# Optimization experiments

Hardware: AMD Instinct MI355X
Metric: run time of the kernel (lower is better)

The kernel has to match this reference:

```python
import jax, jax.numpy as jnp
import numpy as np

HIDDEN = 2048
HEADS = 16
KV_LORA = 512
ROPE_D = 64
NOPE_D = ROPE_D          # module sets qk_nope_head_dim = qk_rope_head_dim
Q_HEAD_D = ROPE_D + NOPE_D
V_D = 128
B, S = 2, 2048
SCALE = ROPE_D ** -0.5


def setup_inputs() -> dict:
    key = jax.random.key(0)
    ks = jax.random.split(key, 6)
    hidden_state = jax.random.normal(ks[0], (B, S, HIDDEN), dtype=jnp.float32)
    attention_mask = jnp.zeros((1, 1, S, S), dtype=jnp.float32)
    s = 0.02
    W_down = jax.random.normal(ks[1], (HIDDEN, KV_LORA + ROPE_D), dtype=jnp.float32) * s
    W_up = jax.random.normal(ks[2], (KV_LORA, HEADS * (NOPE_D + V_D)), dtype=jnp.float32) * s
    W_q = jax.random.normal(ks[3], (HIDDEN, HEADS * Q_HEAD_D), dtype=jnp.float32) * s
    W_o = jax.random.normal(ks[4], (HEADS * V_D, HIDDEN), dtype=jnp.float32) * s
    return {"hidden_state": hidden_state, "attention_mask": attention_mask,
            "W_down": W_down, "W_up": W_up, "W_q": W_q, "W_o": W_o}


def reference(hidden_state, attention_mask, W_down, W_up, W_q, W_o):
    b, s, _ = hidden_state.shape
    # low-rank KV down-projection; split latent and shared rope key
    kv_down = hidden_state @ W_down                      # [b,s,kv_lora+rope]
    kv_compressed = kv_down[..., :KV_LORA]
    k_rope = kv_down[..., KV_LORA:]                      # [b,s,rope]
    # up-project latent to per-head nope-key and value
    kv = (kv_compressed @ W_up).reshape(b, s, HEADS, NOPE_D + V_D)
    kv = kv.transpose(0, 2, 1, 3)                        # [b,h,s,nope+v]
    k_nope = kv[..., :NOPE_D]
    v = kv[..., NOPE_D:]
    # queries
    q = (hidden_state @ W_q).reshape(b, s, HEADS, Q_HEAD_D).transpose(0, 2, 1, 3)
    q_rope = q[..., :ROPE_D]
    q_nope = q[..., ROPE_D:]
    q_full = jnp.concatenate([q_rope, q_nope], axis=-1)  # [b,h,s,2d]
    # broadcast shared rope key across heads and concat with per-head nope key
    k_rope_exp = jnp.broadcast_to(k_rope[:, None], (b, HEADS, s, ROPE_D))
    k_full = jnp.concatenate([k_rope_exp, k_nope], axis=-1)
    scores = jnp.einsum('bhqd,bhkd->bhqk', q_full, k_full) * SCALE
    scores = scores + attention_mask
    probs = jax.nn.softmax(scores, axis=-1)
    ctx = jnp.einsum('bhqk,bhkd->bhqd', probs, v)        # [b,h,s,v]
    ctx = ctx.transpose(0, 2, 1, 3).reshape(b, s, HEADS * V_D)
    return ctx @ W_o
```

## Files before the change

### kernel.cpp

```cpp
#include <hip/hip_runtime.h>
#include <hip/hip_bf16.h>

#define HEADS   16
#define S_LEN   2048
#define BATCH   2
#define MTOT    (BATCH * S_LEN)
#define HIDDEN  2048
#define SCALE   0.125f
#define QKD_LD  2688

typedef __attribute__((ext_vector_type(8))) short          bf16x8;
typedef __attribute__((ext_vector_type(8))) unsigned short u16x8;
typedef __attribute__((ext_vector_type(4))) unsigned short u16x4;
typedef __attribute__((ext_vector_type(4))) float          f32x4;

__device__ __forceinline__ unsigned short f2bf(float f) {
    union { float f; unsigned u; } v; v.f = f;
    unsigned r = v.u + 0x7FFFu + ((v.u >> 16) & 1u);
    return (unsigned short)(r >> 16);
}

__device__ __forceinline__ void gld16(const void* g, const void* l) {
    __builtin_amdgcn_global_load_lds(
        (const __attribute__((address_space(1))) void*)g,
        (__attribute__((address_space(3))) void*)l, 16, 0, 0);
}

__global__ __launch_bounds__(256)
void cast_bf16(const float* __restrict__ in, unsigned short* __restrict__ out)
{
    const size_t i = ((size_t)blockIdx.x * 256 + threadIdx.x) * 8;
    float4 a = *(const float4*)&in[i];
    float4 b = *(const float4*)&in[i + 4];
    u16x8 o;
    o[0] = f2bf(a.x); o[1] = f2bf(a.y); o[2] = f2bf(a.z); o[3] = f2bf(a.w);
    o[4] = f2bf(b.x); o[5] = f2bf(b.y); o[6] = f2bf(b.z); o[7] = f2bf(b.w);
    *(u16x8*)&out[i] = o;
}

__global__ __launch_bounds__(256)
void tc_w(const float* __restrict__ W, int N, int K, unsigned short* __restrict__ Wt)
{
    __shared__ float Tf[64][68];
    const int t  = threadIdx.x;
    const int n0 = blockIdx.x * 64, k0 = blockIdx.y * 64;
    if (n0 >= N) {
        u16x8 z = {0,0,0,0,0,0,0,0};
#pragma unroll
        for (int ii = 0; ii < 2; ii++) {
            int idx = t + 256 * ii;
            int rn = idx >> 3, c8 = (idx & 7) * 8;
            *(u16x8*)&Wt[(size_t)(n0 + rn) * K + k0 + c8] = z;
        }
        return;
    }
#pragma unroll
    for (int ii = 0; ii < 4; ii++) {
        int idx = t + 256 * ii;
        int rk = idx >> 4, c4 = (idx & 15) * 4;
        *(float4*)&Tf[rk][c4] = *(const float4*)&W[(size_t)(k0 + rk) * N + n0 + c4];
    }
    __syncthreads();
#pragma unroll
    for (int ii = 0; ii < 2; ii++) {
        int idx = t + 256 * ii;
        int rn = idx >> 3, c8 = (idx & 7) * 8;
        u16x8 o;
#pragma unroll
        for (int j = 0; j < 8; j++) o[j] = f2bf(Tf[c8 + j][rn]);
        *(u16x8*)&Wt[(size_t)(n0 + rn) * K + k0 + c8] = o;
    }
}

__global__ __launch_bounds__(256)
void transpose_v(const unsigned short* __restrict__ kvu, unsigned short* __restrict__ vT)
{
    __shared__ unsigned short Ts[64][80];
    const int t  = threadIdx.x;
    const int s0 = blockIdx.x * 64;
    const int h  = blockIdx.y >> 1, d0 = (blockIdx.y & 1) * 64;
    const int b  = blockIdx.z;
    const size_t base = (size_t)b * S_LEN;
#pragma unroll
    for (int ii = 0; ii < 2; ii++) {
        int idx = t + 256 * ii;
        int rs = idx >> 3, c8 = (idx & 7) * 8;
        *(u16x8*)&Ts[rs][c8] =
            *(const u16x8*)&kvu[(base + s0 + rs) * 3072 + h * 192 + 64 + d0 + c8];
    }
    __syncthreads();
    const size_t bh = (size_t)(b * HEADS + h);
#pragma unroll
    for (int ii = 0; ii < 2; ii++) {
        int idx = t + 256 * ii;
        int rd = idx >> 3, c8 = (idx & 7) * 8;
        u16x8 o;
#pragma unroll
        for (int j = 0; j < 8; j++) o[j] = Ts[c8 + j][rd];
        *(u16x8*)&vT[(bh * 128 + d0 + rd) * S_LEN + s0 + c8] = o;
    }
}

template<bool OUT_BF16>
__global__ __launch_bounds__(256)
void gemm_bf16(const unsigned short* __restrict__ A, int lda, int K,
               const unsigned short* __restrict__ Bt,
               void* __restrict__ C, int N, int ldc)
{
    __shared__ unsigned short As[128 * 32];
    __shared__ unsigned short Bs[128 * 32];
    const int t = threadIdx.x, lane = t & 63, w = t >> 6;
    const int l15 = lane & 15, lg = lane >> 4;
    const int row0 = blockIdx.y * 128, col0 = blockIdx.x * 128;
    const int wr = w >> 1, wc = w & 1;

    f32x4 acc[4][4] = {};

    for (int k0 = 0; k0 < K; k0 += 32) {
        __syncthreads();
#pragma unroll
        for (int ii = 0; ii < 2; ii++) {
            int u = (ii * 4 + w) * 64 + lane;
            gld16(&A[(size_t)(row0 + (u >> 2)) * lda + k0 + (u & 3) * 8],
                  (char*)As + (ii * 4 + w) * 1024);
            gld16(&Bt[(size_t)(col0 + (u >> 2)) * K + k0 + (u & 3) * 8],
                  (char*)Bs + (ii * 4 + w) * 1024);
        }
        __syncthreads();
        bf16x8 af[4], bb[4];
#pragma unroll
        for (int m = 0; m < 4; m++)
            af[m] = *(const bf16x8*)&As[(wr * 64 + m * 16 + l15) * 32 + lg * 8];
#pragma unroll
        for (int n = 0; n < 4; n++)
            bb[n] = *(const bf16x8*)&Bs[(wc * 64 + n * 16 + l15) * 32 + lg * 8];
#pragma unroll
        for (int m = 0; m < 4; m++)
#pragma unroll
            for (int n = 0; n < 4; n++)
                acc[m][n] = __builtin_amdgcn_mfma_f32_16x16x32_bf16(
                    af[m], bb[n], acc[m][n], 0, 0, 0);
    }

#pragma unroll
    for (int m = 0; m < 4; m++)
#pragma unroll
        for (int n = 0; n < 4; n++) {
            int col = col0 + wc * 64 + n * 16 + l15;
            if (col < N) {
#pragma unroll
                for (int r = 0; r < 4; r++) {
                    int row = row0 + wr * 64 + m * 16 + lg * 4 + r;
                    if (OUT_BF16)
                        ((unsigned short*)C)[(size_t)row * ldc + col] = f2bf(acc[m][n][r]);
                    else
                        ((float*)C)[(size_t)row * ldc + col] = acc[m][n][r];
                }
            }
        }
}

__global__ __launch_bounds__(256, 2)
void mla_attn_mfma(const unsigned short* __restrict__ qkd,
                   const unsigned short* __restrict__ kvu,
                   const unsigned short* __restrict__ vT,
                   const float* __restrict__ mask,
                   unsigned short* __restrict__ ctxb)
{
    __shared__ unsigned short Ks[64 * 128];
    __shared__ unsigned short Vs[128 * 64];
    __shared__ unsigned short Pl[4][32 * 72];
    const int t = threadIdx.x, lane = t & 63, w = t >> 6;
    const int l15 = lane & 15, lg = lane >> 4;
    const int h = blockIdx.y, b = blockIdx.z;
    const int q0 = blockIdx.x * 128 + w * 32;
    const size_t base = (size_t)b * S_LEN;
    const size_t bh = (size_t)(b * HEADS + h);
    const unsigned short* qb = qkd + 640;
    unsigned short* Pw = &Pl[w][0];

    bf16x8 qf[2][4];
#pragma unroll
    for (int m = 0; m < 2; m++)
#pragma unroll
        for (int kk = 0; kk < 4; kk++)
            qf[m][kk] = *(const bf16x8*)&qb[(base + q0 + m * 16 + l15) * QKD_LD
                                            + h * 128 + kk * 32 + lg * 8];

    f32x4 octx[2][8] = {};
    float mrun[2] = {-INFINITY, -INFINITY};
    float lrun[2] = {0.f, 0.f};

    for (int kt = 0; kt < S_LEN / 64; kt++) {
        const int s0 = kt * 64;
        __syncthreads();
#pragma unroll
        for (int ii = 0; ii < 4; ii++) {
            int u = (ii * 4 + w) * 64 + lane;
            {
                int row = u >> 4, x = u & 15, y = x ^ (row & 7);
                const unsigned short* g = (y < 8)
                    ? &qkd[(base + s0 + row) * QKD_LD + 512 + y * 8]
                    : &kvu[(base + s0 + row) * 3072 + h * 192 + (y - 8) * 8];
                gld16(g, (char*)Ks + (ii * 4 + w) * 1024);
            }
            {
                int d = u >> 3, x = u & 7, y = x ^ (d & 7);
                gld16(&vT[(bh * 128 + d) * S_LEN + s0 + y * 8],
                      (char*)Vs + (ii * 4 + w) * 1024);
            }
        }
        __syncthreads();

        f32x4 sc[2][4] = {};
#pragma unroll
        for (int n = 0; n < 4; n++) {
            const int key = n * 16 + l15;
#pragma unroll
            for (int kk = 0; kk < 4; kk++) {
                const int x = (kk * 4 + lg) ^ (key & 7);
                bf16x8 kf = *(const bf16x8*)&Ks[key * 128 + x * 8];
                sc[0][n] = __builtin_amdgcn_mfma_f32_16x16x32_bf16(kf, qf[0][kk], sc[0][n], 0, 0, 0);
                sc[1][n] = __builtin_amdgcn_mfma_f32_16x16x32_bf16(kf, qf[1][kk], sc[1][n], 0, 0, 0);
            }
        }

        float e_bc[2][4];
#pragma unroll
        for (int m = 0; m < 2; m++) {
            const size_t qrow = (size_t)(q0 + m * 16 + l15);
            float sv[4][4];
#pragma unroll
            for (int n = 0; n < 4; n++) {
                float4 mv = *(const float4*)&mask[qrow * S_LEN + s0 + n * 16 + lg * 4];
                sv[n][0] = sc[m][n][0] * SCALE + mv.x;
                sv[n][1] = sc[m][n][1] * SCALE + mv.y;
                sv[n][2] = sc[m][n][2] * SCALE + mv.z;
                sv[n][3] = sc[m][n][3] * SCALE + mv.w;
            }
            float loc = sv[0][0];
#pragma unroll
            for (int n = 0; n < 4; n++)
#pragma unroll
                for (int r = 0; r < 4; r++) loc = fmaxf(loc, sv[n][r]);
            loc = fmaxf(loc, __shfl_xor(loc, 16));
            loc = fmaxf(loc, __shfl_xor(loc, 32));
            float mnew = fmaxf(mrun[m], loc);
            float esc = __expf(mrun[m] - mnew);
            mrun[m] = mnew;
            float ls = 0.f;
#pragma unroll
            for (int n = 0; n < 4; n++) {
                float p0 = __expf(sv[n][0] - mnew), p1 = __expf(sv[n][1] - mnew);
                float p2 = __expf(sv[n][2] - mnew), p3 = __expf(sv[n][3] - mnew);
                ls += (p0 + p1) + (p2 + p3);
                u16x4 pk = { f2bf(p0), f2bf(p1), f2bf(p2), f2bf(p3) };
                *(u16x4*)&Pw[(m * 16 + l15) * 72 + n * 16 + lg * 4] = pk;
            }
            ls += __shfl_xor(ls, 16);
            ls += __shfl_xor(ls, 32);
            lrun[m] = lrun[m] * esc + ls;
#pragma unroll
            for (int r = 0; r < 4; r++) e_bc[m][r] = __shfl(esc, lg * 4 + r);
        }

#pragma unroll
        for (int m = 0; m < 2; m++)
#pragma unroll
            for (int vn = 0; vn < 8; vn++)
#pragma unroll
                for (int r = 0; r < 4; r++) octx[m][vn][r] *= e_bc[m][r];

        asm volatile("" ::: "memory");

        bf16x8 paf[2][2];
#pragma unroll
        for (int m = 0; m < 2; m++)
#pragma unroll
            for (int kk = 0; kk < 2; kk++)
                paf[m][kk] = *(const bf16x8*)&Pw[(m * 16 + l15) * 72 + kk * 32 + lg * 8];
#pragma unroll
        for (int vn = 0; vn < 8; vn++) {
            const int d = vn * 16 + l15;
#pragma unroll
            for (int kk = 0; kk < 2; kk++) {
                const int x = (kk * 4 + lg) ^ (d & 7);
                bf16x8 vf = *(const bf16x8*)&Vs[d * 64 + x * 8];
                octx[0][vn] = __builtin_amdgcn_mfma_f32_16x16x32_bf16(paf[0][kk], vf, octx[0][vn], 0, 0, 0);
                octx[1][vn] = __builtin_amdgcn_mfma_f32_16x16x32_bf16(paf[1][kk], vf, octx[1][vn], 0, 0, 0);
            }
        }
    }

#pragma unroll
    for (int m = 0; m < 2; m++) {
        float inv[4];
#pragma unroll
        for (int r = 0; r < 4; r++) inv[r] = 1.0f / __shfl(lrun[m], lg * 4 + r);
#pragma unroll
        for (int vn = 0; vn < 8; vn++)
#pragma unroll
            for (int r = 0; r < 4; r++)
                ctxb[(base + q0 + m * 16 + lg * 4 + r) * 2048 + h * 128 + vn * 16 + l15]
                    = f2bf(octx[m][vn][r] * inv[r]);
    }
}

extern "C" void kernel_launch(void* const* d_in, const int* in_sizes, int n_in,
                              void* d_out, int out_size, void* d_ws, size_t ws_size,
                              hipStream_t stream)
{
    const float* hidden = (const float*)d_in[0];
    const float* mask   = (const float*)d_in[1];
    const float* W_down = (const float*)d_in[2];
    const float* W_up   = (const float*)d_in[3];
    const float* W_q    = (const float*)d_in[4];
    const float* W_o    = (const float*)d_in[5];
    float* out = (float*)d_out;

    unsigned short* p = (unsigned short*)d_ws;
    unsigned short* hb      = p; p += (size_t)MTOT * 2048;
    unsigned short* qkd     = p; p += (size_t)MTOT * QKD_LD;
    unsigned short* kvu_b   = p; p += (size_t)MTOT * 3072;
    unsigned short* vTb     = p; p += (size_t)BATCH * HEADS * 128 * S_LEN;
    unsigned short* ctxb    = p; p += (size_t)MTOT * 2048;
    unsigned short* Wt_cat  = p; p += (size_t)QKD_LD * 2048;
    unsigned short* Wt_up   = p; p += (size_t)3072 * 512;
    unsigned short* Wt_o    = p; p += (size_t)2048 * 2048;

    dim3 blk(256);
    cast_bf16<<<dim3(MTOT * 2048 / (256 * 8)), blk, 0, stream>>>(hidden, hb);
    tc_w<<<dim3(10, 32), blk, 0, stream>>>(W_down, 576, 2048, Wt_cat);
    tc_w<<<dim3(32, 32), blk, 0, stream>>>(W_q, 2048, 2048, Wt_cat + (size_t)640 * 2048);
    tc_w<<<dim3(48, 8),  blk, 0, stream>>>(W_up, 3072, 512, Wt_up);
    tc_w<<<dim3(32, 32), blk, 0, stream>>>(W_o, 2048, 2048, Wt_o);

    gemm_bf16<true><<<dim3(QKD_LD / 128, 32), blk, 0, stream>>>(
        hb, 2048, 2048, Wt_cat, qkd, QKD_LD, QKD_LD);
    gemm_bf16<true><<<dim3(24, 32), blk, 0, stream>>>(
        qkd, QKD_LD, 512, Wt_up, kvu_b, 3072, 3072);

    transpose_v<<<dim3(S_LEN / 64, 2 * HEADS, BATCH), blk, 0, stream>>>(kvu_b, vTb);

    mla_attn_mfma<<<dim3(S_LEN / 128, HEADS, BATCH), blk, 0, stream>>>(
        qkd, kvu_b, vTb, mask, ctxb);

    gemm_bf16<false><<<dim3(16, 32), blk, 0, stream>>>(
        ctxb, 2048, 2048, Wt_o, out, 2048, 2048);
}
```

Baseline: 302.5 us.

## Double-buffer K/V tiles in attention with async prefetch and swizzled P buffer

```diff
diff --git a/kernel.cpp b/kernel.cpp
--- a/kernel.cpp
+++ b/kernel.cpp
@@ -20,6 +20,12 @@
     return (unsigned short)(r >> 16);
 }
 
+__device__ __forceinline__ unsigned cvtpk(float a, float b) {
+    unsigned r;
+    asm("v_cvt_pk_bf16_f32 %0, %1, %2" : "=v"(r) : "v"(a), "v"(b));
+    return r;
+}
+
 __device__ __forceinline__ void gld16(const void* g, const void* l) {
     __builtin_amdgcn_global_load_lds(
         (const __attribute__((address_space(1))) void*)g,
@@ -167,9 +173,8 @@
                    const float* __restrict__ mask,
                    unsigned short* __restrict__ ctxb)
 {
-    __shared__ unsigned short Ks[64 * 128];
-    __shared__ unsigned short Vs[128 * 64];
-    __shared__ unsigned short Pl[4][32 * 72];
+    __shared__ unsigned short KV[2][64 * 128 + 128 * 64];
+    __shared__ unsigned short Pl[4][32 * 64];
     const int t = threadIdx.x, lane = t & 63, w = t >> 6;
     const int l15 = lane & 15, lg = lane >> 4;
     const int h = blockIdx.y, b = blockIdx.z;
@@ -178,6 +183,7 @@
     const size_t bh = (size_t)(b * HEADS + h);
     const unsigned short* qb = qkd + 640;
     unsigned short* Pw = &Pl[w][0];
+    const unsigned psw = (unsigned)(l15 & 7) << 4;
 
     bf16x8 qf[2][4];
 #pragma unroll
@@ -191,9 +197,12 @@
     float mrun[2] = {-INFINITY, -INFINITY};
     float lrun[2] = {0.f, 0.f};
 
-    for (int kt = 0; kt < S_LEN / 64; kt++) {
-        const int s0 = kt * 64;
-        __syncthreads();
+    const float* mrow0 = &mask[(size_t)(q0 + l15) * S_LEN + lg * 4];
+    const float* mrow1 = mrow0 + (size_t)16 * S_LEN;
+
+    auto STAGE = [&](int buf, int s0) {
+        unsigned short* Kb = &KV[buf][0];
+        unsigned short* Vb = &KV[buf][64 * 128];
 #pragma unroll
         for (int ii = 0; ii < 4; ii++) {
             int u = (ii * 4 + w) * 64 + lane;
@@ -202,17 +211,48 @@
                 const unsigned short* g = (y < 8)
                     ? &qkd[(base + s0 + row) * QKD_LD + 512 + y * 8]
                     : &kvu[(base + s0 + row) * 3072 + h * 192 + (y - 8) * 8];
-                gld16(g, (char*)Ks + (ii * 4 + w) * 1024);
+                gld16(g, (char*)Kb + (ii * 4 + w) * 1024);
             }
             {
                 int d = u >> 3, x = u & 7, y = x ^ (d & 7);
                 gld16(&vT[(bh * 128 + d) * S_LEN + s0 + y * 8],
-                      (char*)Vs + (ii * 4 + w) * 1024);
-            }
-        }
-        __syncthreads();
+                      (char*)Vb + (ii * 4 + w) * 1024);
+            }
+        }
+    };
+
+    const int NT = S_LEN / 64;
+    STAGE(0, 0);
+
+    for (int kt = 0; kt < NT; kt++) {
+        const int cur = kt & 1;
+        const int s0 = kt * 64;
+        const unsigned short* Ks = &KV[cur][0];
+        const unsigned short* Vs = &KV[cur][64 * 128];
+
+        __builtin_amdgcn_s_barrier();
+
+        float4 mv[2][4];
+#pragma unroll
+        for (int n = 0; n < 4; n++) {
+            mv[0][n] = *(const float4*)&mrow0[s0 + n * 16];
+            mv[1][n] = *(const float4*)&mrow1[s0 + n * 16];
+        }
+        __builtin_amdgcn_sched_barrier(0);
+
+        if (kt + 1 < NT) {
+            STAGE(cur ^ 1, s0 + 64);
+            __builtin_amdgcn_sched_barrier(0);
+            asm volatile("s_waitcnt vmcnt(16)" ::: "memory");
+        } else {
+            __builtin_amdgcn_sched_barrier(0);
+            asm volatile("s_waitcnt vmcnt(8)" ::: "memory");
+        }
+        __builtin_amdgcn_sched_barrier(0);
+        __builtin_amdgcn_s_barrier();
 
         f32x4 sc[2][4] = {};
+        __builtin_amdgcn_s_setprio(1);
 #pragma unroll
         for (int n = 0; n < 4; n++) {
             const int key = n * 16 + l15;
@@ -224,19 +264,18 @@
                 sc[1][n] = __builtin_amdgcn_mfma_f32_16x16x32_bf16(kf, qf[1][kk], sc[1][n], 0, 0, 0);
             }
         }
+        __builtin_amdgcn_s_setprio(0);
 
         float e_bc[2][4];
 #pragma unroll
         for (int m = 0; m < 2; m++) {
-            const size_t qrow = (size_t)(q0 + m * 16 + l15);
             float sv[4][4];
 #pragma unroll
             for (int n = 0; n < 4; n++) {
-                float4 mv = *(const float4*)&mask[qrow * S_LEN + s0 + n * 16 + lg * 4];
-                sv[n][0] = sc[m][n][0] * SCALE + mv.x;
-                sv[n][1] = sc[m][n][1] * SCALE + mv.y;
-                sv[n][2] = sc[m][n][2] * SCALE + mv.z;
-                sv[n][3] = sc[m][n][3] * SCALE + mv.w;
+                sv[n][0] = sc[m][n][0] * SCALE + mv[m][n].x;
+                sv[n][1] = sc[m][n][1] * SCALE + mv[m][n].y;
+                sv[n][2] = sc[m][n][2] * SCALE + mv[m][n].z;
+                sv[n][3] = sc[m][n][3] * SCALE + mv[m][n].w;
             }
             float loc = sv[0][0];
 #pragma unroll
@@ -249,13 +288,16 @@
             float esc = __expf(mrun[m] - mnew);
             mrun[m] = mnew;
             float ls = 0.f;
+            const int prow = m * 16 + l15;
 #pragma unroll
             for (int n = 0; n < 4; n++) {
                 float p0 = __expf(sv[n][0] - mnew), p1 = __expf(sv[n][1] - mnew);
                 float p2 = __expf(sv[n][2] - mnew), p3 = __expf(sv[n][3] - mnew);
                 ls += (p0 + p1) + (p2 + p3);
-                u16x4 pk = { f2bf(p0), f2bf(p1), f2bf(p2), f2bf(p3) };
-                *(u16x4*)&Pw[(m * 16 + l15) * 72 + n * 16 + lg * 4] = pk;
+                union { unsigned u[2]; u16x4 v; } pk;
+                pk.u[0] = cvtpk(p0, p1);
+                pk.u[1] = cvtpk(p2, p3);
+                *(u16x4*)((char*)Pw + prow * 128 + ((n * 32 + lg * 8) ^ psw)) = pk.v;
             }
             ls += __shfl_xor(ls, 16);
             ls += __shfl_xor(ls, 32);
@@ -275,10 +317,14 @@
 
         bf16x8 paf[2][2];
 #pragma unroll
-        for (int m = 0; m < 2; m++)
+        for (int m = 0; m < 2; m++) {
+            const int prow = m * 16 + l15;
 #pragma unroll
             for (int kk = 0; kk < 2; kk++)
-                paf[m][kk] = *(const bf16x8*)&Pw[(m * 16 + l15) * 72 + kk * 32 + lg * 8];
+                paf[m][kk] = *(const bf16x8*)((char*)Pw + prow * 128
+                                              + ((kk * 64 + lg * 16) ^ psw));
+        }
+        __builtin_amdgcn_s_setprio(1);
 #pragma unroll
         for (int vn = 0; vn < 8; vn++) {
             const int d = vn * 16 + l15;
@@ -290,6 +336,7 @@
                 octx[1][vn] = __builtin_amdgcn_mfma_f32_16x16x32_bf16(paf[1][kk], vf, octx[1][vn], 0, 0, 0);
             }
         }
+        __builtin_amdgcn_s_setprio(0);
     }
 
 #pragma unroll
```

New measurement: 297.5 us. No clear change (-1.6%).

## Shrink attention query tile, add lazy rescale, packed bf16 convert, and MFMA priority

Applied to the files above, without the earlier changes.

```diff
diff --git a/kernel.cpp b/kernel.cpp
--- a/kernel.cpp
+++ b/kernel.cpp
@@ -20,6 +20,12 @@
     return (unsigned short)(r >> 16);
 }
 
+__device__ __forceinline__ unsigned cvtpk(float a, float b) {
+    unsigned r;
+    asm("v_cvt_pk_bf16_f32 %0, %1, %2" : "=v"(r) : "v"(a), "v"(b));
+    return r;
+}
+
 __device__ __forceinline__ void gld16(const void* g, const void* l) {
     __builtin_amdgcn_global_load_lds(
         (const __attribute__((address_space(1))) void*)g,
@@ -160,7 +166,7 @@
         }
 }
 
-__global__ __launch_bounds__(256, 2)
+__global__ __launch_bounds__(256, 4)
 void mla_attn_mfma(const unsigned short* __restrict__ qkd,
                    const unsigned short* __restrict__ kvu,
                    const unsigned short* __restrict__ vT,
@@ -169,31 +175,34 @@
 {
     __shared__ unsigned short Ks[64 * 128];
     __shared__ unsigned short Vs[128 * 64];
-    __shared__ unsigned short Pl[4][32 * 72];
+    __shared__ unsigned short Pl[4][16 * 64];
     const int t = threadIdx.x, lane = t & 63, w = t >> 6;
     const int l15 = lane & 15, lg = lane >> 4;
     const int h = blockIdx.y, b = blockIdx.z;
-    const int q0 = blockIdx.x * 128 + w * 32;
+    const int q0 = blockIdx.x * 64 + w * 16;
     const size_t base = (size_t)b * S_LEN;
     const size_t bh = (size_t)(b * HEADS + h);
     const unsigned short* qb = qkd + 640;
     unsigned short* Pw = &Pl[w][0];
-
-    bf16x8 qf[2][4];
-#pragma unroll
-    for (int m = 0; m < 2; m++)
-#pragma unroll
-        for (int kk = 0; kk < 4; kk++)
-            qf[m][kk] = *(const bf16x8*)&qb[(base + q0 + m * 16 + l15) * QKD_LD
-                                            + h * 128 + kk * 32 + lg * 8];
-
-    f32x4 octx[2][8] = {};
-    float mrun[2] = {-INFINITY, -INFINITY};
-    float lrun[2] = {0.f, 0.f};
-
-    for (int kt = 0; kt < S_LEN / 64; kt++) {
+    const unsigned psw = (unsigned)(l15 & 7) << 4;
+
+    bf16x8 qf[4];
+#pragma unroll
+    for (int kk = 0; kk < 4; kk++)
+        qf[kk] = *(const bf16x8*)&qb[(base + q0 + l15) * QKD_LD
+                                     + h * 128 + kk * 32 + lg * 8];
+
+    f32x4 octx[8] = {};
+    float mrun = -INFINITY, lrun = 0.f;
+
+    const float* mrow = &mask[(size_t)(q0 + l15) * S_LEN + lg * 4];
+
+    const int NT = S_LEN / 64;
+    for (int kt = 0; kt < NT; kt++) {
         const int s0 = kt * 64;
-        __syncthreads();
+
+        __builtin_amdgcn_s_barrier();
+
 #pragma unroll
         for (int ii = 0; ii < 4; ii++) {
             int u = (ii * 4 + w) * 64 + lane;
@@ -210,9 +219,17 @@
                       (char*)Vs + (ii * 4 + w) * 1024);
             }
         }
-        __syncthreads();
-
-        f32x4 sc[2][4] = {};
+        __builtin_amdgcn_sched_barrier(0);
+
+        float4 mv[4];
+#pragma unroll
+        for (int n = 0; n < 4; n++) mv[n] = *(const float4*)&mrow[s0 + n * 16];
+        __builtin_amdgcn_sched_barrier(0);
+        asm volatile("s_waitcnt vmcnt(4)" ::: "memory");
+        __builtin_amdgcn_s_barrier();
+
+        f32x4 sc[4] = {};
+        __builtin_amdgcn_s_setprio(1);
 #pragma unroll
         for (int n = 0; n < 4; n++) {
             const int key = n * 16 + l15;
@@ -220,65 +237,63 @@
             for (int kk = 0; kk < 4; kk++) {
                 const int x = (kk * 4 + lg) ^ (key & 7);
                 bf16x8 kf = *(const bf16x8*)&Ks[key * 128 + x * 8];
-                sc[0][n] = __builtin_amdgcn_mfma_f32_16x16x32_bf16(kf, qf[0][kk], sc[0][n], 0, 0, 0);
-                sc[1][n] = __builtin_amdgcn_mfma_f32_16x16x32_bf16(kf, qf[1][kk], sc[1][n], 0, 0, 0);
-            }
-        }
-
-        float e_bc[2][4];
-#pragma unroll
-        for (int m = 0; m < 2; m++) {
-            const size_t qrow = (size_t)(q0 + m * 16 + l15);
-            float sv[4][4];
-#pragma unroll
-            for (int n = 0; n < 4; n++) {
-                float4 mv = *(const float4*)&mask[qrow * S_LEN + s0 + n * 16 + lg * 4];
-                sv[n][0] = sc[m][n][0] * SCALE + mv.x;
-                sv[n][1] = sc[m][n][1] * SCALE + mv.y;
-                sv[n][2] = sc[m][n][2] * SCALE + mv.z;
-                sv[n][3] = sc[m][n][3] * SCALE + mv.w;
-            }
-            float loc = sv[0][0];
-#pragma unroll
-            for (int n = 0; n < 4; n++)
-#pragma unroll
-                for (int r = 0; r < 4; r++) loc = fmaxf(loc, sv[n][r]);
-            loc = fmaxf(loc, __shfl_xor(loc, 16));
-            loc = fmaxf(loc, __shfl_xor(loc, 32));
-            float mnew = fmaxf(mrun[m], loc);
-            float esc = __expf(mrun[m] - mnew);
-            mrun[m] = mnew;
-            float ls = 0.f;
-#pragma unroll
-            for (int n = 0; n < 4; n++) {
-                float p0 = __expf(sv[n][0] - mnew), p1 = __expf(sv[n][1] - mnew);
-                float p2 = __expf(sv[n][2] - mnew), p3 = __expf(sv[n][3] - mnew);
-                ls += (p0 + p1) + (p2 + p3);
-                u16x4 pk = { f2bf(p0), f2bf(p1), f2bf(p2), f2bf(p3) };
-                *(u16x4*)&Pw[(m * 16 + l15) * 72 + n * 16 + lg * 4] = pk;
-            }
-            ls += __shfl_xor(ls, 16);
-            ls += __shfl_xor(ls, 32);
-            lrun[m] = lrun[m] * esc + ls;
-#pragma unroll
-            for (int r = 0; r < 4; r++) e_bc[m][r] = __shfl(esc, lg * 4 + r);
-        }
-
-#pragma unroll
-        for (int m = 0; m < 2; m++)
+                sc[n] = __builtin_amdgcn_mfma_f32_16x16x32_bf16(kf, qf[kk], sc[n], 0, 0, 0);
+            }
+        }
+        __builtin_amdgcn_s_setprio(0);
+
+        float sv[4][4];
+#pragma unroll
+        for (int n = 0; n < 4; n++) {
+            sv[n][0] = sc[n][0] * SCALE + mv[n].x;
+            sv[n][1] = sc[n][1] * SCALE + mv[n].y;
+            sv[n][2] = sc[n][2] * SCALE + mv[n].z;
+            sv[n][3] = sc[n][3] * SCALE + mv[n].w;
+        }
+        float loc = sv[0][0];
+#pragma unroll
+        for (int n = 0; n < 4; n++)
+#pragma unroll
+            for (int r = 0; r < 4; r++) loc = fmaxf(loc, sv[n][r]);
+        loc = fmaxf(loc, __shfl_xor(loc, 16));
+        loc = fmaxf(loc, __shfl_xor(loc, 32));
+
+        if (!__all((int)(loc <= mrun + 8.f))) {
+            float mnew = fmaxf(mrun, loc);
+            float esc = __expf(mrun - mnew);
+            mrun = mnew;
+            lrun *= esc;
+            float e_bc[4];
+#pragma unroll
+            for (int r = 0; r < 4; r++) e_bc[r] = __shfl(esc, lg * 4 + r);
 #pragma unroll
             for (int vn = 0; vn < 8; vn++)
 #pragma unroll
-                for (int r = 0; r < 4; r++) octx[m][vn][r] *= e_bc[m][r];
+                for (int r = 0; r < 4; r++) octx[vn][r] *= e_bc[r];
+        }
+
+        float ls = 0.f;
+#pragma unroll
+        for (int n = 0; n < 4; n++) {
+            float p0 = __expf(sv[n][0] - mrun), p1 = __expf(sv[n][1] - mrun);
+            float p2 = __expf(sv[n][2] - mrun), p3 = __expf(sv[n][3] - mrun);
+            ls += (p0 + p1) + (p2 + p3);
+            union { unsigned u[2]; u16x4 v; } pk;
+            pk.u[0] = cvtpk(p0, p1);
+            pk.u[1] = cvtpk(p2, p3);
+            *(u16x4*)((char*)Pw + l15 * 128 + ((n * 32 + lg * 8) ^ psw)) = pk.v;
+        }
+        ls += __shfl_xor(ls, 16);
+        ls += __shfl_xor(ls, 32);
+        lrun += ls;
 
         asm volatile("" ::: "memory");
 
-        bf16x8 paf[2][2];
-#pragma unroll
-        for (int m = 0; m < 2; m++)
-#pragma unroll
-            for (int kk = 0; kk < 2; kk++)
-                paf[m][kk] = *(const bf16x8*)&Pw[(m * 16 + l15) * 72 + kk * 32 + lg * 8];
+        bf16x8 paf[2];
+#pragma unroll
+        for (int kk = 0; kk < 2; kk++)
+            paf[kk] = *(const bf16x8*)((char*)Pw + l15 * 128 + ((kk * 64 + lg * 16) ^ psw));
+        __builtin_amdgcn_s_setprio(1);
 #pragma unroll
         for (int vn = 0; vn < 8; vn++) {
             const int d = vn * 16 + l15;
@@ -286,24 +301,21 @@
             for (int kk = 0; kk < 2; kk++) {
                 const int x = (kk * 4 + lg) ^ (d & 7);
                 bf16x8 vf = *(const bf16x8*)&Vs[d * 64 + x * 8];
-                octx[0][vn] = __builtin_amdgcn_mfma_f32_16x16x32_bf16(paf[0][kk], vf, octx[0][vn], 0, 0, 0);
-                octx[1][vn] = __builtin_amdgcn_mfma_f32_16x16x32_bf16(paf[1][kk], vf, octx[1][vn], 0, 0, 0);
-            }
-        }
-    }
-
-#pragma unroll
-    for (int m = 0; m < 2; m++) {
-        float inv[4];
-#pragma unroll
-        for (int r = 0; r < 4; r++) inv[r] = 1.0f / __shfl(lrun[m], lg * 4 + r);
-#pragma unroll
-        for (int vn = 0; vn < 8; vn++)
-#pragma unroll
-            for (int r = 0; r < 4; r++)
-                ctxb[(base + q0 + m * 16 + lg * 4 + r) * 2048 + h * 128 + vn * 16 + l15]
-                    = f2bf(octx[m][vn][r] * inv[r]);
-    }
+                octx[vn] = __builtin_amdgcn_mfma_f32_16x16x32_bf16(paf[kk], vf, octx[vn], 0, 0, 0);
+            }
+        }
+        __builtin_amdgcn_s_setprio(0);
+    }
+
+    float inv[4];
+#pragma unroll
+    for (int r = 0; r < 4; r++) inv[r] = 1.0f / __shfl(lrun, lg * 4 + r);
+#pragma unroll
+    for (int vn = 0; vn < 8; vn++)
+#pragma unroll
+        for (int r = 0; r < 4; r++)
+            ctxb[(base + q0 + lg * 4 + r) * 2048 + h * 128 + vn * 16 + l15]
+                = f2bf(octx[vn][r] * inv[r]);
 }
 
 extern "C" void kernel_launch(void* const* d_in, const int* in_sizes, int n_in,
@@ -342,7 +354,7 @@
 
     transpose_v<<<dim3(S_LEN / 64, 2 * HEADS, BATCH), blk, 0, stream>>>(kvu_b, vTb);
 
-    mla_attn_mfma<<<dim3(S_LEN / 128, HEADS, BATCH), blk, 0, stream>>>(
+    mla_attn_mfma<<<dim3(S_LEN / 64, HEADS, BATCH), blk, 0, stream>>>(
         qkd, kvu_b, vTb, mask, ctxb);
 
     gemm_bf16<false><<<dim3(16, 32), blk, 0, stream>>>(
```

New measurement: 334.2 us. 10.5% more time.
